# Performance work log

Hardware: AMD Instinct MI355X
Metric: run time of the kernel (lower is better)

Reference implementation:

```python
import jax, jax.numpy as jnp
import numpy as np

EPS = 1e-9


def setup_inputs() -> dict:
    key = jax.random.key(0)
    k1, k2, k3 = jax.random.split(key, 3)
    B, N, E, F_IN, F_OUT = 8, 2048, 1024, 256, 256
    x = jax.random.normal(k1, (B, N, F_IN), dtype=jnp.float32)
    H = jax.random.uniform(k2, (B, N, E), dtype=jnp.float32)  # soft incidence matrix
    weight = jax.random.normal(k3, (F_IN, F_OUT), dtype=jnp.float32) * (1.0 / np.sqrt(F_OUT))
    return {"x": x, "H": H, "weight": weight}


def reference(x, H, weight):
    # x: [B, N, Fin], H: [B, N, E], weight: [Fin, Fout]
    # Torch builds diag_embed(Dv_inv)/diag_embed(De_inv) and uses dense bmm;
    # mathematically identical to elementwise row-scaling, done here directly.
    Dv = jnp.sum(H, axis=2)                       # [B, N]  (= bmm(H, ones))
    De = jnp.sum(H, axis=1)                       # [B, E]
    Dv_inv = 1.0 / (Dv + EPS)
    De_inv = 1.0 / (De + EPS)
    xw = jnp.matmul(x, weight)                    # [B, N, Fout]
    HTX = jnp.einsum('bne,bnf->bef', H, xw)       # H^T @ X
    HDeHTX = jnp.einsum('bne,bef->bnf', H, De_inv[:, :, None] * HTX)
    out = Dv_inv[:, :, None] * HDeHTX             # [B, N, Fout]
    # dropout in eval mode (identity); relu kept
    return jax.nn.relu(out)
```

## Files before the change

### kernel.cpp

```cpp
#include <hip/hip_runtime.h>
#include <stdint.h>


typedef __bf16 bf16x8 __attribute__((ext_vector_type(8)));
typedef float f32x4 __attribute__((ext_vector_type(4)));

#define PADK 72

__device__ __forceinline__ uint16_t f2b(float f) {
  __bf16 h = (__bf16)f;
  return __builtin_bit_cast(uint16_t, h);
}

__device__ __forceinline__ f32x4 mfma16(bf16x8 a, bf16x8 b, f32x4 c) {
  return __builtin_amdgcn_mfma_f32_16x16x32_bf16(a, b, c, 0, 0, 0);
}

__device__ __forceinline__ void gload16(const void* src, void* dst) {
  __builtin_amdgcn_global_load_lds(
      (const __attribute__((address_space(1))) void*)src,
      (__attribute__((address_space(3))) void*)dst, 16, 0, 0);
}

#define PIPE_WAIT4() do { \
    asm volatile("s_waitcnt vmcnt(4)" ::: "memory"); \
    __builtin_amdgcn_s_barrier(); \
    __builtin_amdgcn_sched_barrier(0); \
  } while (0)
#define PIPE_WAIT0() do { \
    asm volatile("s_waitcnt vmcnt(0)" ::: "memory"); \
    __builtin_amdgcn_s_barrier(); \
    __builtin_amdgcn_sched_barrier(0); \
  } while (0)

__global__ __launch_bounds__(256) void k_prep_w(const float* __restrict__ W,
    uint16_t* __restrict__ Wt) {
  __shared__ __align__(16) uint16_t T[64 * 68];
  const int k0 = blockIdx.x * 64, f0 = blockIdx.y * 64;
  const int t = threadIdx.x;
  const int r0 = (t >> 4) * 4, cc = (t & 15) * 4;
  float vv[4][4];
  #pragma unroll
  for (int i = 0; i < 4; ++i) {
    float4 q = *(const float4*)(W + (size_t)(k0 + r0 + i) * 256 + f0 + cc);
    vv[i][0] = q.x; vv[i][1] = q.y; vv[i][2] = q.z; vv[i][3] = q.w;
  }
  #pragma unroll
  for (int j = 0; j < 4; ++j) {
    union { uint16_t s[4]; uint2 u; } p;
    #pragma unroll
    for (int i = 0; i < 4; ++i) p.s[i] = f2b(vv[i][j]);
    *(uint2*)&T[(cc + j) * 68 + r0] = p.u;
  }
  __syncthreads();
  const int er = t >> 2, c2 = (t & 3) * 16;
  union { uint16_t s[16]; uint4 q[2]; } o;
  #pragma unroll
  for (int m = 0; m < 4; ++m)
    *(uint2*)&o.s[m * 4] = *(const uint2*)&T[er * 68 + c2 + m * 4];
  uint16_t* dst = Wt + (size_t)(f0 + er) * 256 + k0 + c2;
  *(uint4*)dst = o.q[0];
  *(uint4*)(dst + 8) = o.q[1];
}

__global__ __launch_bounds__(256) void k_phase1(const float* __restrict__ H,
    const float* __restrict__ X, const uint16_t* __restrict__ Wt,
    uint16_t* __restrict__ Hbt, uint16_t* __restrict__ Hb,
    float* __restrict__ DvPart, float* __restrict__ DePart,
    uint16_t* __restrict__ XWt) {
  __shared__ __align__(16) unsigned char smem[25600];
  const int lin = blockIdx.x;
  const int t = threadIdx.x, lane = t & 63, wave = t >> 6;

  if (lin < 512) {
    uint16_t* As = (uint16_t*)smem;
    uint16_t* Bs = (uint16_t*)(smem + 16384);
    const int n0 = (lin & 31) * 64, f0 = ((lin >> 5) & 1) * 128, b = lin >> 6;
    const int l15 = lane & 15, lq = lane >> 4;
    const int rlane = lane >> 3;
    const int srcswz = ((lane & 7) ^ rlane) << 3;
    const uint16_t* Ag = Wt + (size_t)f0 * 256;
    const int br = t >> 2, kc = (t & 3) * 16;
    const float* Xg = X + ((size_t)b * 2048 + n0 + br) * 256 + kc;
    f32x4 acc[4][2] = {};
    for (int kt = 0; kt < 4; ++kt) {
      if (kt) __syncthreads();
      const int k0 = kt * 64;
      #pragma unroll
      for (int i = 0; i < 4; ++i) {
        const int r = wave * 32 + i * 8;
        gload16(Ag + (size_t)(r + rlane) * 256 + k0 + srcswz, As + r * 64);
      }
      {
        float4 RX[4];
        const float* s = Xg + k0;
        #pragma unroll
        for (int q = 0; q < 4; ++q) RX[q] = *(const float4*)(s + q * 4);
        uint16_t* d = Bs + br * PADK + kc;
        const float* f = (const float*)RX;
        #pragma unroll
        for (int q = 0; q < 2; ++q) {
          union { uint16_t s[8]; uint4 u; } p;
          #pragma unroll
          for (int j = 0; j < 8; ++j) p.s[j] = f2b(f[q * 8 + j]);
          *(uint4*)(d + q * 8) = p.u;
        }
      }
      __syncthreads();
      #pragma unroll
      for (int h = 0; h < 2; ++h) {
        bf16x8 af[4], bf[2];
        #pragma unroll
        for (int i = 0; i < 4; ++i) {
          const int r = (wave >> 1) * 64 + i * 16 + l15;
          af[i] = *(const bf16x8*)(As + r * 64 + ((((h << 2) | lq) ^ (r & 7)) << 3));
        }
        #pragma unroll
        for (int j = 0; j < 2; ++j) {
          const int r = (wave & 1) * 32 + j * 16 + l15;
          bf[j] = *(const bf16x8*)(Bs + r * PADK + h * 32 + lq * 8);
        }
        #pragma unroll
        for (int i = 0; i < 4; ++i)
          #pragma unroll
          for (int j = 0; j < 2; ++j)
            acc[i][j] = mfma16(af[i], bf[j], acc[i][j]);
      }
    }
    #pragma unroll
    for (int i = 0; i < 4; ++i) {
      const int fr = f0 + (wave >> 1) * 64 + i * 16 + lq * 4;
      #pragma unroll
      for (int j = 0; j < 2; ++j) {
        const int col = n0 + (wave & 1) * 32 + j * 16 + l15;
        #pragma unroll
        for (int reg = 0; reg < 4; ++reg)
          XWt[((size_t)b * 256 + fr + reg) * 2048 + col] = f2b(acc[i][j][reg]);
      }
    }
  } else {
    uint16_t* T = (uint16_t*)smem;
    float* cs = (float*)(smem + 8704);
    const int l2 = lin - 512;
    const int n0 = (l2 & 31) * 64, e0 = ((l2 >> 5) & 15) * 64, b = l2 >> 9;
    const int r0 = (t >> 4) * 4;
    const int cc = (t & 15) * 4;
    float vv[4][4];
    float dv[4];
    float de0 = 0.f, de1 = 0.f, de2 = 0.f, de3 = 0.f;
    #pragma unroll
    for (int i = 0; i < 4; ++i) {
      float4 q = *(const float4*)(H + ((size_t)b * 2048 + n0 + r0 + i) * 1024 + e0 + cc);
      vv[i][0] = q.x; vv[i][1] = q.y; vv[i][2] = q.z; vv[i][3] = q.w;
      float rs = (q.x + q.y) + (q.z + q.w);
      rs += __shfl_xor(rs, 1); rs += __shfl_xor(rs, 2);
      rs += __shfl_xor(rs, 4); rs += __shfl_xor(rs, 8);
      dv[i] = rs;
      de0 += q.x; de1 += q.y; de2 += q.z; de3 += q.w;
    }
    #pragma unroll
    for (int i = 0; i < 4; ++i) {
      union { uint16_t s[4]; uint2 u; } p;
      #pragma unroll
      for (int j = 0; j < 4; ++j) p.s[j] = f2b(vv[i][j]);
      *(uint2*)(Hb + ((size_t)b * 2048 + n0 + r0 + i) * 1024 + e0 + cc) = p.u;
    }
    #pragma unroll
    for (int j = 0; j < 4; ++j) {
      union { uint16_t s[4]; uint2 u; } p;
      #pragma unroll
      for (int i = 0; i < 4; ++i) p.s[i] = f2b(vv[i][j]);
      *(uint2*)&T[(cc + j) * 68 + r0] = p.u;
    }
    de0 += __shfl_xor(de0, 16); de0 += __shfl_xor(de0, 32);
    de1 += __shfl_xor(de1, 16); de1 += __shfl_xor(de1, 32);
    de2 += __shfl_xor(de2, 16); de2 += __shfl_xor(de2, 32);
    de3 += __shfl_xor(de3, 16); de3 += __shfl_xor(de3, 32);
    if (lane < 16) *(float4*)&cs[wave * 64 + cc] = make_float4(de0, de1, de2, de3);
    if ((lane & 15) == 0) {
      #pragma unroll
      for (int i = 0; i < 4; ++i)
        DvPart[((size_t)b * 2048 + n0 + r0 + i) * 16 + ((l2 >> 5) & 15)] = dv[i];
    }
    __syncthreads();
    const int er = t >> 2, c2 = (t & 3) * 16;
    union { uint16_t s[16]; uint4 q[2]; } o;
    #pragma unroll
    for (int m = 0; m < 4; ++m)
      *(uint2*)&o.s[m * 4] = *(const uint2*)&T[er * 68 + c2 + m * 4];
    uint16_t* dst = Hbt + ((size_t)b * 1024 + e0 + er) * 2048 + n0 + c2;
    *(uint4*)dst = o.q[0];
    *(uint4*)(dst + 8) = o.q[1];
    if (t < 64) {
      float s = (cs[0 * 64 + t] + cs[1 * 64 + t]) + (cs[2 * 64 + t] + cs[3 * 64 + t]);
      DePart[((size_t)b * 1024 + e0 + t) * 32 + (l2 & 31)] = s;
    }
  }
}

__global__ __launch_bounds__(256) void k_gemm2(const uint16_t* __restrict__ Hbt,
    const uint16_t* __restrict__ XWt, const float* __restrict__ DePart,
    uint16_t* __restrict__ Yt) {
  __shared__ __align__(16) uint16_t As[3][64 * 64];
  __shared__ __align__(16) uint16_t Bs[3][64 * 64];
  __shared__ float sde[64];
  const int e0 = blockIdx.x * 64, f0 = blockIdx.y * 64, b = blockIdx.z;
  const int t = threadIdx.x, lane = t & 63, wave = t >> 6;
  const int l15 = lane & 15, lq = lane >> 4;
  const int rlane = lane >> 3;
  const int srcswz = ((lane & 7) ^ rlane) << 3;
  const uint16_t* Ag = XWt + ((size_t)b * 256 + f0) * 2048;
  const uint16_t* Bg = Hbt + ((size_t)b * 1024 + e0) * 2048;
  auto stage = [&](uint16_t* Ad, uint16_t* Bd, int kt) {
    const int k0 = kt * 64;
    #pragma unroll
    for (int i = 0; i < 2; ++i) {
      const int r = wave * 16 + i * 8;
      gload16(Ag + (size_t)(r + rlane) * 2048 + k0 + srcswz, Ad + r * 64);
      gload16(Bg + (size_t)(r + rlane) * 2048 + k0 + srcswz, Bd + r * 64);
    }
  };
  f32x4 acc[2][2] = {};
  auto compute = [&](const uint16_t* Ad, const uint16_t* Bd) {
    #pragma unroll
    for (int h = 0; h < 2; ++h) {
      bf16x8 af[2], bf[2];
      #pragma unroll
      for (int i = 0; i < 2; ++i) {
        const int r = (wave >> 1) * 32 + i * 16 + l15;
        af[i] = *(const bf16x8*)(Ad + r * 64 + ((((h << 2) | lq) ^ (r & 7)) << 3));
      }
      #pragma unroll
      for (int j = 0; j < 2; ++j) {
        const int r = (wave & 1) * 32 + j * 16 + l15;
        bf[j] = *(const bf16x8*)(Bd + r * 64 + ((((h << 2) | lq) ^ (r & 7)) << 3));
      }
      #pragma unroll
      for (int i = 0; i < 2; ++i)
        #pragma unroll
        for (int j = 0; j < 2; ++j)
          acc[i][j] = mfma16(af[i], bf[j], acc[i][j]);
    }
  };
  if (t < 64) {
    const float* p = DePart + ((size_t)b * 1024 + e0 + t) * 32;
    float4 a0 = *(const float4*)(p + 0),  a1 = *(const float4*)(p + 4);
    float4 a2 = *(const float4*)(p + 8),  a3 = *(const float4*)(p + 12);
    float4 a4 = *(const float4*)(p + 16), a5 = *(const float4*)(p + 20);
    float4 a6 = *(const float4*)(p + 24), a7 = *(const float4*)(p + 28);
    float s = (((a0.x + a0.y) + (a0.z + a0.w)) + ((a1.x + a1.y) + (a1.z + a1.w)))
            + (((a2.x + a2.y) + (a2.z + a2.w)) + ((a3.x + a3.y) + (a3.z + a3.w)))
            + ((((a4.x + a4.y) + (a4.z + a4.w)) + ((a5.x + a5.y) + (a5.z + a5.w)))
            + (((a6.x + a6.y) + (a6.z + a6.w)) + ((a7.x + a7.y) + (a7.z + a7.w))));
    sde[t] = 1.f / (s + 1e-9f);
  }
  stage(As[0], Bs[0], 0);
  stage(As[1], Bs[1], 1);
  __syncthreads();
  const int NT = 32;
  uint16_t *cA = As[0], *nA = As[1], *fA = As[2];
  uint16_t *cB = Bs[0], *nB = Bs[1], *fB = Bs[2];
  for (int kt = 0; kt < NT - 2; ++kt) {
    stage(fA, fB, kt + 2);
    compute(cA, cB);
    PIPE_WAIT4();
    uint16_t* t1 = cA; cA = nA; nA = fA; fA = t1;
    uint16_t* t2 = cB; cB = nB; nB = fB; fB = t2;
  }
  compute(cA, cB);
  PIPE_WAIT0();
  compute(nA, nB);
  #pragma unroll
  for (int i = 0; i < 2; ++i) {
    const int fr = f0 + (wave >> 1) * 32 + i * 16 + lq * 4;
    #pragma unroll
    for (int j = 0; j < 2; ++j) {
      const int el = (wave & 1) * 32 + j * 16 + l15;
      const float sc = sde[el];
      uint16_t* dst = Yt + ((size_t)b * 256 + fr) * 1024 + e0 + el;
      #pragma unroll
      for (int reg = 0; reg < 4; ++reg)
        dst[(size_t)reg * 1024] = f2b(acc[i][j][reg] * sc);
    }
  }
}

__global__ __launch_bounds__(256) void k_gemm3(const uint16_t* __restrict__ Hb,
    const uint16_t* __restrict__ Yt, const float* __restrict__ DvPart,
    float* __restrict__ out) {
  __shared__ __align__(16) uint16_t As[3][64 * 64];
  __shared__ __align__(16) uint16_t Bs[3][64 * 64];
  __shared__ float sdv[64];
  const int n0 = blockIdx.x * 64, f0 = blockIdx.y * 64, b = blockIdx.z;
  const int t = threadIdx.x, lane = t & 63, wave = t >> 6;
  const int l15 = lane & 15, lq = lane >> 4;
  const int rlane = lane >> 3;
  const int srcswz = ((lane & 7) ^ rlane) << 3;
  const uint16_t* Ag = Hb + ((size_t)b * 2048 + n0) * 1024;
  const uint16_t* Bg = Yt + ((size_t)b * 256 + f0) * 1024;
  auto stage = [&](uint16_t* Ad, uint16_t* Bd, int kt) {
    const int k0 = kt * 64;
    #pragma unroll
    for (int i = 0; i < 2; ++i) {
      const int r = wave * 16 + i * 8;
      gload16(Ag + (size_t)(r + rlane) * 1024 + k0 + srcswz, Ad + r * 64);
      gload16(Bg + (size_t)(r + rlane) * 1024 + k0 + srcswz, Bd + r * 64);
    }
  };
  f32x4 acc[2][2] = {};
  auto compute = [&](const uint16_t* Ad, const uint16_t* Bd) {
    #pragma unroll
    for (int h = 0; h < 2; ++h) {
      bf16x8 af[2], bf[2];
      #pragma unroll
      for (int i = 0; i < 2; ++i) {
        const int r = (wave >> 1) * 32 + i * 16 + l15;
        af[i] = *(const bf16x8*)(Ad + r * 64 + ((((h << 2) | lq) ^ (r & 7)) << 3));
      }
      #pragma unroll
      for (int j = 0; j < 2; ++j) {
        const int r = (wave & 1) * 32 + j * 16 + l15;
        bf[j] = *(const bf16x8*)(Bd + r * 64 + ((((h << 2) | lq) ^ (r & 7)) << 3));
      }
      #pragma unroll
      for (int i = 0; i < 2; ++i)
        #pragma unroll
        for (int j = 0; j < 2; ++j)
          acc[i][j] = mfma16(af[i], bf[j], acc[i][j]);
    }
  };
  if (t < 64) {
    const float* p = DvPart + ((size_t)b * 2048 + n0 + t) * 16;
    float4 a0 = *(const float4*)(p + 0),  a1 = *(const float4*)(p + 4);
    float4 a2 = *(const float4*)(p + 8),  a3 = *(const float4*)(p + 12);
    float s = (((a0.x + a0.y) + (a0.z + a0.w)) + ((a1.x + a1.y) + (a1.z + a1.w)))
            + (((a2.x + a2.y) + (a2.z + a2.w)) + ((a3.x + a3.y) + (a3.z + a3.w)));
    sdv[t] = 1.f / (s + 1e-9f);
  }
  stage(As[0], Bs[0], 0);
  stage(As[1], Bs[1], 1);
  __syncthreads();
  const int NT = 16;
  uint16_t *cA = As[0], *nA = As[1], *fA = As[2];
  uint16_t *cB = Bs[0], *nB = Bs[1], *fB = Bs[2];
  for (int kt = 0; kt < NT - 2; ++kt) {
    stage(fA, fB, kt + 2);
    compute(cA, cB);
    PIPE_WAIT4();
    uint16_t* t1 = cA; cA = nA; nA = fA; fA = t1;
    uint16_t* t2 = cB; cB = nB; nB = fB; fB = t2;
  }
  compute(cA, cB);
  PIPE_WAIT0();
  compute(nA, nB);
  #pragma unroll
  for (int i = 0; i < 2; ++i) {
    const int nl = (wave >> 1) * 32 + i * 16 + lq * 4;
    #pragma unroll
    for (int reg = 0; reg < 4; ++reg) {
      const int row = n0 + nl + reg;
      const float sc = sdv[nl + reg];
      #pragma unroll
      for (int j = 0; j < 2; ++j) {
        const int col = f0 + (wave & 1) * 32 + j * 16 + l15;
        const float v = acc[i][j][reg] * sc;
        out[((size_t)b * 2048 + row) * 256 + col] = v > 0.f ? v : 0.f;
      }
    }
  }
}

extern "C" void kernel_launch(void* const* d_in, const int* in_sizes, int n_in,
                              void* d_out, int out_size, void* d_ws, size_t ws_size,
                              hipStream_t stream) {
  (void)in_sizes; (void)n_in; (void)out_size;
  const float* x = (const float*)d_in[0];
  const float* H = (const float*)d_in[1];
  const float* W = (const float*)d_in[2];
  float* out = (float*)d_out;

  if (ws_size < 81920000) return;
  char* ws = (char*)d_ws;
  uint16_t* Hbt    = (uint16_t*)(ws);
  uint16_t* Hb     = (uint16_t*)(ws + 33554432);
  uint16_t* XWt    = (uint16_t*)(ws + 67108864);
  uint16_t* Yt     = (uint16_t*)(ws + 75497472);
  float*    DvPart = (float*)(ws + 79691776);
  float*    DePart = (float*)(ws + 80740352);
  uint16_t* Wt     = (uint16_t*)(ws + 81788928);

  k_prep_w<<<dim3(4, 4),     256, 0, stream>>>(W, Wt);
  k_phase1<<<dim3(4608),     256, 0, stream>>>(H, x, Wt, Hbt, Hb, DvPart, DePart, XWt);
  k_gemm2 <<<dim3(16, 4, 8), 256, 0, stream>>>(Hbt, XWt, DePart, Yt);
  k_gemm3 <<<dim3(32, 4, 8), 256, 0, stream>>>(Hb, Yt, DvPart, out);
}
```

Before: 76.46 us.

## Rebalance phase1: H blocks process two E tiles, XW GEMM tiles shrink

The fused phase-1 kernel now schedules the H conversion blocks first, and each one handles two 64-wide E tiles (128 columns). That halves the H block count and the Dv partial count, so k_gemm3 reads 8 partials instead of 16. The XW GEMM blocks shrink from 128x64 to 64x64 output tiles, doubling their count to 1024 and cutting LDS use. The goal is better load balance, with the memory-bound H work launched first and less per-block overhead. The cost is higher register pressure in the H path and more redundant X loads in the GEMM.

Result: no change. 77.01 us (+0.7%).

```diff
diff --git a/kernel.cpp b/kernel.cpp
--- a/kernel.cpp
+++ b/kernel.cpp
@@ -4,8 +4,6 @@
 
 typedef __bf16 bf16x8 __attribute__((ext_vector_type(8)));
 typedef float f32x4 __attribute__((ext_vector_type(4)));
-
-#define PADK 72
 
 __device__ __forceinline__ uint16_t f2b(float f) {
   __bf16 h = (__bf16)f;
@@ -68,27 +66,131 @@
     uint16_t* __restrict__ Hbt, uint16_t* __restrict__ Hb,
     float* __restrict__ DvPart, float* __restrict__ DePart,
     uint16_t* __restrict__ XWt) {
-  __shared__ __align__(16) unsigned char smem[25600];
+  __shared__ __align__(16) unsigned char smem[20480];
   const int lin = blockIdx.x;
   const int t = threadIdx.x, lane = t & 63, wave = t >> 6;
 
-  if (lin < 512) {
+  if (lin < 2048) {
+    uint16_t* T0 = (uint16_t*)smem;
+    uint16_t* T1 = (uint16_t*)(smem + 9216);
+    float* cs = (float*)(smem + 18432);
+    const int n0 = (lin & 31) * 64, ep = (lin >> 5) & 7, b = lin >> 8;
+    const int e0a = ep * 128, e0b = e0a + 64;
+    const int r0 = (t >> 4) * 4;
+    const int cc = (t & 15) * 4;
+    float4 q0[4], q1[4];
+    #pragma unroll
+    for (int i = 0; i < 4; ++i)
+      q0[i] = *(const float4*)(H + ((size_t)b * 2048 + n0 + r0 + i) * 1024 + e0a + cc);
+    #pragma unroll
+    for (int i = 0; i < 4; ++i)
+      q1[i] = *(const float4*)(H + ((size_t)b * 2048 + n0 + r0 + i) * 1024 + e0b + cc);
+    float dv[4];
+    {
+      float de0 = 0.f, de1 = 0.f, de2 = 0.f, de3 = 0.f;
+      #pragma unroll
+      for (int i = 0; i < 4; ++i) {
+        float4 q = q0[i];
+        float rs = (q.x + q.y) + (q.z + q.w);
+        rs += __shfl_xor(rs, 1); rs += __shfl_xor(rs, 2);
+        rs += __shfl_xor(rs, 4); rs += __shfl_xor(rs, 8);
+        dv[i] = rs;
+        de0 += q.x; de1 += q.y; de2 += q.z; de3 += q.w;
+        union { uint16_t s[4]; uint2 u; } p;
+        p.s[0] = f2b(q.x); p.s[1] = f2b(q.y); p.s[2] = f2b(q.z); p.s[3] = f2b(q.w);
+        *(uint2*)(Hb + ((size_t)b * 2048 + n0 + r0 + i) * 1024 + e0a + cc) = p.u;
+      }
+      #pragma unroll
+      for (int j = 0; j < 4; ++j) {
+        union { uint16_t s[4]; uint2 u; } p;
+        p.s[0] = f2b(((const float*)&q0[0])[j]);
+        p.s[1] = f2b(((const float*)&q0[1])[j]);
+        p.s[2] = f2b(((const float*)&q0[2])[j]);
+        p.s[3] = f2b(((const float*)&q0[3])[j]);
+        *(uint2*)&T0[(cc + j) * 72 + r0] = p.u;
+      }
+      de0 += __shfl_xor(de0, 16); de0 += __shfl_xor(de0, 32);
+      de1 += __shfl_xor(de1, 16); de1 += __shfl_xor(de1, 32);
+      de2 += __shfl_xor(de2, 16); de2 += __shfl_xor(de2, 32);
+      de3 += __shfl_xor(de3, 16); de3 += __shfl_xor(de3, 32);
+      if (lane < 16) *(float4*)&cs[(0 * 4 + wave) * 64 + cc] = make_float4(de0, de1, de2, de3);
+    }
+    {
+      float de0 = 0.f, de1 = 0.f, de2 = 0.f, de3 = 0.f;
+      #pragma unroll
+      for (int i = 0; i < 4; ++i) {
+        float4 q = q1[i];
+        float rs = (q.x + q.y) + (q.z + q.w);
+        rs += __shfl_xor(rs, 1); rs += __shfl_xor(rs, 2);
+        rs += __shfl_xor(rs, 4); rs += __shfl_xor(rs, 8);
+        dv[i] += rs;
+        de0 += q.x; de1 += q.y; de2 += q.z; de3 += q.w;
+        union { uint16_t s[4]; uint2 u; } p;
+        p.s[0] = f2b(q.x); p.s[1] = f2b(q.y); p.s[2] = f2b(q.z); p.s[3] = f2b(q.w);
+        *(uint2*)(Hb + ((size_t)b * 2048 + n0 + r0 + i) * 1024 + e0b + cc) = p.u;
+      }
+      #pragma unroll
+      for (int j = 0; j < 4; ++j) {
+        union { uint16_t s[4]; uint2 u; } p;
+        p.s[0] = f2b(((const float*)&q1[0])[j]);
+        p.s[1] = f2b(((const float*)&q1[1])[j]);
+        p.s[2] = f2b(((const float*)&q1[2])[j]);
+        p.s[3] = f2b(((const float*)&q1[3])[j]);
+        *(uint2*)&T1[(cc + j) * 72 + r0] = p.u;
+      }
+      de0 += __shfl_xor(de0, 16); de0 += __shfl_xor(de0, 32);
+      de1 += __shfl_xor(de1, 16); de1 += __shfl_xor(de1, 32);
+      de2 += __shfl_xor(de2, 16); de2 += __shfl_xor(de2, 32);
+      de3 += __shfl_xor(de3, 16); de3 += __shfl_xor(de3, 32);
+      if (lane < 16) *(float4*)&cs[(1 * 4 + wave) * 64 + cc] = make_float4(de0, de1, de2, de3);
+    }
+    if ((lane & 15) == 0) {
+      #pragma unroll
+      for (int i = 0; i < 4; ++i)
+        DvPart[((size_t)b * 2048 + n0 + r0 + i) * 8 + ep] = dv[i];
+    }
+    __syncthreads();
+    const int er = t >> 2, c2 = (t & 3) * 16;
+    {
+      uint4 o0 = *(const uint4*)&T0[er * 72 + c2];
+      uint4 o1 = *(const uint4*)&T0[er * 72 + c2 + 8];
+      uint16_t* dst = Hbt + ((size_t)b * 1024 + e0a + er) * 2048 + n0 + c2;
+      *(uint4*)dst = o0;
+      *(uint4*)(dst + 8) = o1;
+    }
+    {
+      uint4 o0 = *(const uint4*)&T1[er * 72 + c2];
+      uint4 o1 = *(const uint4*)&T1[er * 72 + c2 + 8];
+      uint16_t* dst = Hbt + ((size_t)b * 1024 + e0b + er) * 2048 + n0 + c2;
+      *(uint4*)dst = o0;
+      *(uint4*)(dst + 8) = o1;
+    }
+    if (t < 64) {
+      float s = (cs[0 * 64 + t] + cs[1 * 64 + t]) + (cs[2 * 64 + t] + cs[3 * 64 + t]);
+      DePart[((size_t)b * 1024 + e0a + t) * 32 + (lin & 31)] = s;
+    } else if (t < 128) {
+      const int t2 = t - 64;
+      float s = (cs[4 * 64 + t2] + cs[5 * 64 + t2]) + (cs[6 * 64 + t2] + cs[7 * 64 + t2]);
+      DePart[((size_t)b * 1024 + e0b + t2) * 32 + (lin & 31)] = s;
+    }
+  } else {
     uint16_t* As = (uint16_t*)smem;
-    uint16_t* Bs = (uint16_t*)(smem + 16384);
-    const int n0 = (lin & 31) * 64, f0 = ((lin >> 5) & 1) * 128, b = lin >> 6;
+    uint16_t* Bs = (uint16_t*)(smem + 8192);
+    const int l1 = lin - 2048;
+    const int n0 = (l1 & 31) * 64, f0 = ((l1 >> 5) & 3) * 64, b = l1 >> 7;
     const int l15 = lane & 15, lq = lane >> 4;
     const int rlane = lane >> 3;
     const int srcswz = ((lane & 7) ^ rlane) << 3;
     const uint16_t* Ag = Wt + (size_t)f0 * 256;
     const int br = t >> 2, kc = (t & 3) * 16;
     const float* Xg = X + ((size_t)b * 2048 + n0 + br) * 256 + kc;
-    f32x4 acc[4][2] = {};
+    f32x4 acc[2][2] = {};
     for (int kt = 0; kt < 4; ++kt) {
       if (kt) __syncthreads();
       const int k0 = kt * 64;
       #pragma unroll
-      for (int i = 0; i < 4; ++i) {
-        const int r = wave * 32 + i * 8;
+      for (int i = 0; i < 2; ++i) {
+        const int r = wave * 16 + i * 8;
         gload16(Ag + (size_t)(r + rlane) * 256 + k0 + srcswz, As + r * 64);
       }
       {
@@ -96,7 +198,7 @@
         const float* s = Xg + k0;
         #pragma unroll
         for (int q = 0; q < 4; ++q) RX[q] = *(const float4*)(s + q * 4);
-        uint16_t* d = Bs + br * PADK + kc;
+        uint16_t* d = Bs + br * 72 + kc;
         const float* f = (const float*)RX;
         #pragma unroll
         for (int q = 0; q < 2; ++q) {
@@ -109,27 +211,27 @@
       __syncthreads();
       #pragma unroll
       for (int h = 0; h < 2; ++h) {
-        bf16x8 af[4], bf[2];
-        #pragma unroll
-        for (int i = 0; i < 4; ++i) {
-          const int r = (wave >> 1) * 64 + i * 16 + l15;
+        bf16x8 af[2], bf[2];
+        #pragma unroll
+        for (int i = 0; i < 2; ++i) {
+          const int r = (wave >> 1) * 32 + i * 16 + l15;
           af[i] = *(const bf16x8*)(As + r * 64 + ((((h << 2) | lq) ^ (r & 7)) << 3));
         }
         #pragma unroll
         for (int j = 0; j < 2; ++j) {
           const int r = (wave & 1) * 32 + j * 16 + l15;
-          bf[j] = *(const bf16x8*)(Bs + r * PADK + h * 32 + lq * 8);
+          bf[j] = *(const bf16x8*)(Bs + r * 72 + h * 32 + lq * 8);
         }
         #pragma unroll
-        for (int i = 0; i < 4; ++i)
+        for (int i = 0; i < 2; ++i)
           #pragma unroll
           for (int j = 0; j < 2; ++j)
             acc[i][j] = mfma16(af[i], bf[j], acc[i][j]);
       }
     }
     #pragma unroll
-    for (int i = 0; i < 4; ++i) {
-      const int fr = f0 + (wave >> 1) * 64 + i * 16 + lq * 4;
+    for (int i = 0; i < 2; ++i) {
+      const int fr = f0 + (wave >> 1) * 32 + i * 16 + lq * 4;
       #pragma unroll
       for (int j = 0; j < 2; ++j) {
         const int col = n0 + (wave & 1) * 32 + j * 16 + l15;
@@ -137,63 +239,6 @@
         for (int reg = 0; reg < 4; ++reg)
           XWt[((size_t)b * 256 + fr + reg) * 2048 + col] = f2b(acc[i][j][reg]);
       }
-    }
-  } else {
-    uint16_t* T = (uint16_t*)smem;
-    float* cs = (float*)(smem + 8704);
-    const int l2 = lin - 512;
-    const int n0 = (l2 & 31) * 64, e0 = ((l2 >> 5) & 15) * 64, b = l2 >> 9;
-    const int r0 = (t >> 4) * 4;
-    const int cc = (t & 15) * 4;
-    float vv[4][4];
-    float dv[4];
-    float de0 = 0.f, de1 = 0.f, de2 = 0.f, de3 = 0.f;
-    #pragma unroll
-    for (int i = 0; i < 4; ++i) {
-      float4 q = *(const float4*)(H + ((size_t)b * 2048 + n0 + r0 + i) * 1024 + e0 + cc);
-      vv[i][0] = q.x; vv[i][1] = q.y; vv[i][2] = q.z; vv[i][3] = q.w;
-      float rs = (q.x + q.y) + (q.z + q.w);
-      rs += __shfl_xor(rs, 1); rs += __shfl_xor(rs, 2);
-      rs += __shfl_xor(rs, 4); rs += __shfl_xor(rs, 8);
-      dv[i] = rs;
-      de0 += q.x; de1 += q.y; de2 += q.z; de3 += q.w;
-    }
-    #pragma unroll
-    for (int i = 0; i < 4; ++i) {
-      union { uint16_t s[4]; uint2 u; } p;
-      #pragma unroll
-      for (int j = 0; j < 4; ++j) p.s[j] = f2b(vv[i][j]);
-      *(uint2*)(Hb + ((size_t)b * 2048 + n0 + r0 + i) * 1024 + e0 + cc) = p.u;
-    }
-    #pragma unroll
-    for (int j = 0; j < 4; ++j) {
-      union { uint16_t s[4]; uint2 u; } p;
-      #pragma unroll
-      for (int i = 0; i < 4; ++i) p.s[i] = f2b(vv[i][j]);
-      *(uint2*)&T[(cc + j) * 68 + r0] = p.u;
-    }
-    de0 += __shfl_xor(de0, 16); de0 += __shfl_xor(de0, 32);
-    de1 += __shfl_xor(de1, 16); de1 += __shfl_xor(de1, 32);
-    de2 += __shfl_xor(de2, 16); de2 += __shfl_xor(de2, 32);
-    de3 += __shfl_xor(de3, 16); de3 += __shfl_xor(de3, 32);
-    if (lane < 16) *(float4*)&cs[wave * 64 + cc] = make_float4(de0, de1, de2, de3);
-    if ((lane & 15) == 0) {
-      #pragma unroll
-      for (int i = 0; i < 4; ++i)
-        DvPart[((size_t)b * 2048 + n0 + r0 + i) * 16 + ((l2 >> 5) & 15)] = dv[i];
-    }
-    __syncthreads();
-    const int er = t >> 2, c2 = (t & 3) * 16;
-    union { uint16_t s[16]; uint4 q[2]; } o;
-    #pragma unroll
-    for (int m = 0; m < 4; ++m)
-      *(uint2*)&o.s[m * 4] = *(const uint2*)&T[er * 68 + c2 + m * 4];
-    uint16_t* dst = Hbt + ((size_t)b * 1024 + e0 + er) * 2048 + n0 + c2;
-    *(uint4*)dst = o.q[0];
-    *(uint4*)(dst + 8) = o.q[1];
-    if (t < 64) {
-      float s = (cs[0 * 64 + t] + cs[1 * 64 + t]) + (cs[2 * 64 + t] + cs[3 * 64 + t]);
-      DePart[((size_t)b * 1024 + e0 + t) * 32 + (l2 & 31)] = s;
     }
   }
 }
@@ -330,11 +375,9 @@
     }
   };
   if (t < 64) {
-    const float* p = DvPart + ((size_t)b * 2048 + n0 + t) * 16;
-    float4 a0 = *(const float4*)(p + 0),  a1 = *(const float4*)(p + 4);
-    float4 a2 = *(const float4*)(p + 8),  a3 = *(const float4*)(p + 12);
-    float s = (((a0.x + a0.y) + (a0.z + a0.w)) + ((a1.x + a1.y) + (a1.z + a1.w)))
-            + (((a2.x + a2.y) + (a2.z + a2.w)) + ((a3.x + a3.y) + (a3.z + a3.w)));
+    const float* p = DvPart + ((size_t)b * 2048 + n0 + t) * 8;
+    float4 a0 = *(const float4*)(p + 0), a1 = *(const float4*)(p + 4);
+    float s = (((a0.x + a0.y) + (a0.z + a0.w)) + ((a1.x + a1.y) + (a1.z + a1.w)));
     sdv[t] = 1.f / (s + 1e-9f);
   }
   stage(As[0], Bs[0], 0);
@@ -390,7 +433,7 @@
   uint16_t* Wt     = (uint16_t*)(ws + 81788928);
 
   k_prep_w<<<dim3(4, 4),     256, 0, stream>>>(W, Wt);
-  k_phase1<<<dim3(4608),     256, 0, stream>>>(H, x, Wt, Hbt, Hb, DvPart, DePart, XWt);
+  k_phase1<<<dim3(3072),     256, 0, stream>>>(H, x, Wt, Hbt, Hb, DvPart, DePart, XWt);
   k_gemm2 <<<dim3(16, 4, 8), 256, 0, stream>>>(Hbt, XWt, DePart, Yt);
   k_gemm3 <<<dim3(32, 4, 8), 256, 0, stream>>>(Hb, Yt, DvPart, out);
 }
```

## Drop transposed H copy; transpose H tiles in LDS inside gemm2

Applied to the files above, without the earlier changes.

Phase1 no longer writes a transposed bf16 copy of H. It streams H in row blocks, writing only Hb, and computes the final DvInv directly along with per-block De partials. gemm2 now reads Hb row-major through registers and transposes each tile into padded LDS, with a register double-buffered pipeline driven by explicit waitcnt and barriers. The XW GEMM is retiled to 64x64 blocks. This saves 32MB of global writes and the workspace, at the cost of extra LDS transpose work and narrower 8-byte loads in gemm2.

After: 88.44 us. 15.7% more time.

```diff
diff --git a/kernel.cpp b/kernel.cpp
--- a/kernel.cpp
+++ b/kernel.cpp
@@ -4,8 +4,6 @@
 
 typedef __bf16 bf16x8 __attribute__((ext_vector_type(8)));
 typedef float f32x4 __attribute__((ext_vector_type(4)));
-
-#define PADK 72
 
 __device__ __forceinline__ uint16_t f2b(float f) {
   __bf16 h = (__bf16)f;
@@ -65,30 +63,61 @@
 
 __global__ __launch_bounds__(256) void k_phase1(const float* __restrict__ H,
     const float* __restrict__ X, const uint16_t* __restrict__ Wt,
-    uint16_t* __restrict__ Hbt, uint16_t* __restrict__ Hb,
-    float* __restrict__ DvPart, float* __restrict__ DePart,
-    uint16_t* __restrict__ XWt) {
-  __shared__ __align__(16) unsigned char smem[25600];
+    uint16_t* __restrict__ Hb, float* __restrict__ DvInv,
+    float* __restrict__ DePart, uint16_t* __restrict__ XWt) {
+  __shared__ __align__(16) unsigned char smem[17408];
   const int lin = blockIdx.x;
   const int t = threadIdx.x, lane = t & 63, wave = t >> 6;
 
-  if (lin < 512) {
+  if (lin < 1024) {
+    float* dvp = (float*)smem;
+    const int nb = lin & 127, b = lin >> 7;
+    const int n0 = nb * 16;
+    const float* Hrow = H + ((size_t)b * 2048 + n0) * 1024 + t * 4;
+    uint16_t* HbRow = Hb + ((size_t)b * 2048 + n0) * 1024 + t * 4;
+    float de0 = 0.f, de1 = 0.f, de2 = 0.f, de3 = 0.f;
+    float4 qn = *(const float4*)(Hrow);
+    #pragma unroll
+    for (int i = 0; i < 16; ++i) {
+      float4 q = qn;
+      if (i < 15) qn = *(const float4*)(Hrow + (size_t)(i + 1) * 1024);
+      de0 += q.x; de1 += q.y; de2 += q.z; de3 += q.w;
+      float rs = (q.x + q.y) + (q.z + q.w);
+      rs += __shfl_xor(rs, 1);  rs += __shfl_xor(rs, 2);
+      rs += __shfl_xor(rs, 4);  rs += __shfl_xor(rs, 8);
+      rs += __shfl_xor(rs, 16); rs += __shfl_xor(rs, 32);
+      if (lane == 0) dvp[i * 4 + wave] = rs;
+      union { uint16_t s[4]; uint2 u; } p;
+      p.s[0] = f2b(q.x); p.s[1] = f2b(q.y); p.s[2] = f2b(q.z); p.s[3] = f2b(q.w);
+      *(uint2*)(HbRow + (size_t)i * 1024) = p.u;
+    }
+    {
+      float* dp = DePart + ((size_t)b * 1024 + t * 4) * 128 + nb;
+      dp[0] = de0; dp[128] = de1; dp[256] = de2; dp[384] = de3;
+    }
+    __syncthreads();
+    if (t < 16) {
+      float s = (dvp[t * 4 + 0] + dvp[t * 4 + 1]) + (dvp[t * 4 + 2] + dvp[t * 4 + 3]);
+      DvInv[b * 2048 + n0 + t] = 1.f / (s + 1e-9f);
+    }
+  } else {
     uint16_t* As = (uint16_t*)smem;
-    uint16_t* Bs = (uint16_t*)(smem + 16384);
-    const int n0 = (lin & 31) * 64, f0 = ((lin >> 5) & 1) * 128, b = lin >> 6;
+    uint16_t* Bs = (uint16_t*)(smem + 8192);
+    const int l1 = lin - 1024;
+    const int n0 = (l1 & 31) * 64, f0 = ((l1 >> 5) & 3) * 64, b = l1 >> 7;
     const int l15 = lane & 15, lq = lane >> 4;
     const int rlane = lane >> 3;
     const int srcswz = ((lane & 7) ^ rlane) << 3;
     const uint16_t* Ag = Wt + (size_t)f0 * 256;
     const int br = t >> 2, kc = (t & 3) * 16;
     const float* Xg = X + ((size_t)b * 2048 + n0 + br) * 256 + kc;
-    f32x4 acc[4][2] = {};
+    f32x4 acc[2][2] = {};
     for (int kt = 0; kt < 4; ++kt) {
       if (kt) __syncthreads();
       const int k0 = kt * 64;
       #pragma unroll
-      for (int i = 0; i < 4; ++i) {
-        const int r = wave * 32 + i * 8;
+      for (int i = 0; i < 2; ++i) {
+        const int r = wave * 16 + i * 8;
         gload16(Ag + (size_t)(r + rlane) * 256 + k0 + srcswz, As + r * 64);
       }
       {
@@ -96,7 +125,7 @@
         const float* s = Xg + k0;
         #pragma unroll
         for (int q = 0; q < 4; ++q) RX[q] = *(const float4*)(s + q * 4);
-        uint16_t* d = Bs + br * PADK + kc;
+        uint16_t* d = Bs + br * 72 + kc;
         const float* f = (const float*)RX;
         #pragma unroll
         for (int q = 0; q < 2; ++q) {
@@ -109,27 +138,27 @@
       __syncthreads();
       #pragma unroll
       for (int h = 0; h < 2; ++h) {
-        bf16x8 af[4], bf[2];
-        #pragma unroll
-        for (int i = 0; i < 4; ++i) {
-          const int r = (wave >> 1) * 64 + i * 16 + l15;
+        bf16x8 af[2], bf[2];
+        #pragma unroll
+        for (int i = 0; i < 2; ++i) {
+          const int r = (wave >> 1) * 32 + i * 16 + l15;
           af[i] = *(const bf16x8*)(As + r * 64 + ((((h << 2) | lq) ^ (r & 7)) << 3));
         }
         #pragma unroll
         for (int j = 0; j < 2; ++j) {
           const int r = (wave & 1) * 32 + j * 16 + l15;
-          bf[j] = *(const bf16x8*)(Bs + r * PADK + h * 32 + lq * 8);
+          bf[j] = *(const bf16x8*)(Bs + r * 72 + h * 32 + lq * 8);
         }
         #pragma unroll
-        for (int i = 0; i < 4; ++i)
+        for (int i = 0; i < 2; ++i)
           #pragma unroll
           for (int j = 0; j < 2; ++j)
             acc[i][j] = mfma16(af[i], bf[j], acc[i][j]);
       }
     }
     #pragma unroll
-    for (int i = 0; i < 4; ++i) {
-      const int fr = f0 + (wave >> 1) * 64 + i * 16 + lq * 4;
+    for (int i = 0; i < 2; ++i) {
+      const int fr = f0 + (wave >> 1) * 32 + i * 16 + lq * 4;
       #pragma unroll
       for (int j = 0; j < 2; ++j) {
         const int col = n0 + (wave & 1) * 32 + j * 16 + l15;
@@ -138,71 +167,15 @@
           XWt[((size_t)b * 256 + fr + reg) * 2048 + col] = f2b(acc[i][j][reg]);
       }
     }
-  } else {
-    uint16_t* T = (uint16_t*)smem;
-    float* cs = (float*)(smem + 8704);
-    const int l2 = lin - 512;
-    const int n0 = (l2 & 31) * 64, e0 = ((l2 >> 5) & 15) * 64, b = l2 >> 9;
-    const int r0 = (t >> 4) * 4;
-    const int cc = (t & 15) * 4;
-    float vv[4][4];
-    float dv[4];
-    float de0 = 0.f, de1 = 0.f, de2 = 0.f, de3 = 0.f;
-    #pragma unroll
-    for (int i = 0; i < 4; ++i) {
-      float4 q = *(const float4*)(H + ((size_t)b * 2048 + n0 + r0 + i) * 1024 + e0 + cc);
-      vv[i][0] = q.x; vv[i][1] = q.y; vv[i][2] = q.z; vv[i][3] = q.w;
-      float rs = (q.x + q.y) + (q.z + q.w);
-      rs += __shfl_xor(rs, 1); rs += __shfl_xor(rs, 2);
-      rs += __shfl_xor(rs, 4); rs += __shfl_xor(rs, 8);
-      dv[i] = rs;
-      de0 += q.x; de1 += q.y; de2 += q.z; de3 += q.w;
-    }
-    #pragma unroll
-    for (int i = 0; i < 4; ++i) {
-      union { uint16_t s[4]; uint2 u; } p;
-      #pragma unroll
-      for (int j = 0; j < 4; ++j) p.s[j] = f2b(vv[i][j]);
-      *(uint2*)(Hb + ((size_t)b * 2048 + n0 + r0 + i) * 1024 + e0 + cc) = p.u;
-    }
-    #pragma unroll
-    for (int j = 0; j < 4; ++j) {
-      union { uint16_t s[4]; uint2 u; } p;
-      #pragma unroll
-      for (int i = 0; i < 4; ++i) p.s[i] = f2b(vv[i][j]);
-      *(uint2*)&T[(cc + j) * 68 + r0] = p.u;
-    }
-    de0 += __shfl_xor(de0, 16); de0 += __shfl_xor(de0, 32);
-    de1 += __shfl_xor(de1, 16); de1 += __shfl_xor(de1, 32);
-    de2 += __shfl_xor(de2, 16); de2 += __shfl_xor(de2, 32);
-    de3 += __shfl_xor(de3, 16); de3 += __shfl_xor(de3, 32);
-    if (lane < 16) *(float4*)&cs[wave * 64 + cc] = make_float4(de0, de1, de2, de3);
-    if ((lane & 15) == 0) {
-      #pragma unroll
-      for (int i = 0; i < 4; ++i)
-        DvPart[((size_t)b * 2048 + n0 + r0 + i) * 16 + ((l2 >> 5) & 15)] = dv[i];
-    }
-    __syncthreads();
-    const int er = t >> 2, c2 = (t & 3) * 16;
-    union { uint16_t s[16]; uint4 q[2]; } o;
-    #pragma unroll
-    for (int m = 0; m < 4; ++m)
-      *(uint2*)&o.s[m * 4] = *(const uint2*)&T[er * 68 + c2 + m * 4];
-    uint16_t* dst = Hbt + ((size_t)b * 1024 + e0 + er) * 2048 + n0 + c2;
-    *(uint4*)dst = o.q[0];
-    *(uint4*)(dst + 8) = o.q[1];
-    if (t < 64) {
-      float s = (cs[0 * 64 + t] + cs[1 * 64 + t]) + (cs[2 * 64 + t] + cs[3 * 64 + t]);
-      DePart[((size_t)b * 1024 + e0 + t) * 32 + (l2 & 31)] = s;
-    }
-  }
-}
-
-__global__ __launch_bounds__(256) void k_gemm2(const uint16_t* __restrict__ Hbt,
+  }
+}
+
+__global__ __launch_bounds__(256) void k_gemm2(const uint16_t* __restrict__ Hb,
     const uint16_t* __restrict__ XWt, const float* __restrict__ DePart,
     uint16_t* __restrict__ Yt) {
   __shared__ __align__(16) uint16_t As[3][64 * 64];
-  __shared__ __align__(16) uint16_t Bs[3][64 * 64];
+  __shared__ __align__(16) uint16_t Bsm[2][64 * 72];
+  __shared__ float sde4[64][4];
   __shared__ float sde[64];
   const int e0 = blockIdx.x * 64, f0 = blockIdx.y * 64, b = blockIdx.z;
   const int t = threadIdx.x, lane = t & 63, wave = t >> 6;
@@ -210,14 +183,29 @@
   const int rlane = lane >> 3;
   const int srcswz = ((lane & 7) ^ rlane) << 3;
   const uint16_t* Ag = XWt + ((size_t)b * 256 + f0) * 2048;
-  const uint16_t* Bg = Hbt + ((size_t)b * 1024 + e0) * 2048;
-  auto stage = [&](uint16_t* Ad, uint16_t* Bd, int kt) {
+  const int br0 = (t >> 4) * 4;
+  const int bcc = (t & 15) * 4;
+  const uint16_t* Bgb = Hb + (size_t)b * 2048 * 1024 + e0 + bcc;
+  auto stageA = [&](uint16_t* Ad, int kt) {
     const int k0 = kt * 64;
     #pragma unroll
     for (int i = 0; i < 2; ++i) {
       const int r = wave * 16 + i * 8;
       gload16(Ag + (size_t)(r + rlane) * 2048 + k0 + srcswz, Ad + r * 64);
-      gload16(Bg + (size_t)(r + rlane) * 2048 + k0 + srcswz, Bd + r * 64);
+    }
+  };
+  auto loadB = [&](uint2* R, int kt) {
+    const uint16_t* s = Bgb + (size_t)(kt * 64 + br0) * 1024;
+    #pragma unroll
+    for (int i = 0; i < 4; ++i) R[i] = *(const uint2*)(s + (size_t)i * 1024);
+  };
+  auto writeB = [&](uint16_t* Bd, const uint2* R) {
+    #pragma unroll
+    for (int j = 0; j < 4; ++j) {
+      union { uint16_t s[4]; uint2 u; } p;
+      #pragma unroll
+      for (int i = 0; i < 4; ++i) p.s[i] = ((const uint16_t*)&R[i])[j];
+      *(uint2*)&Bd[(bcc + j) * 72 + br0] = p.u;
     }
   };
   f32x4 acc[2][2] = {};
@@ -233,7 +221,7 @@
       #pragma unroll
       for (int j = 0; j < 2; ++j) {
         const int r = (wave & 1) * 32 + j * 16 + l15;
-        bf[j] = *(const bf16x8*)(Bd + r * 64 + ((((h << 2) | lq) ^ (r & 7)) << 3));
+        bf[j] = *(const bf16x8*)(Bd + r * 72 + h * 32 + lq * 8);
       }
       #pragma unroll
       for (int i = 0; i < 2; ++i)
@@ -242,34 +230,54 @@
           acc[i][j] = mfma16(af[i], bf[j], acc[i][j]);
     }
   };
-  if (t < 64) {
-    const float* p = DePart + ((size_t)b * 1024 + e0 + t) * 32;
-    float4 a0 = *(const float4*)(p + 0),  a1 = *(const float4*)(p + 4);
-    float4 a2 = *(const float4*)(p + 8),  a3 = *(const float4*)(p + 12);
-    float4 a4 = *(const float4*)(p + 16), a5 = *(const float4*)(p + 20);
-    float4 a6 = *(const float4*)(p + 24), a7 = *(const float4*)(p + 28);
-    float s = (((a0.x + a0.y) + (a0.z + a0.w)) + ((a1.x + a1.y) + (a1.z + a1.w)))
-            + (((a2.x + a2.y) + (a2.z + a2.w)) + ((a3.x + a3.y) + (a3.z + a3.w)))
-            + ((((a4.x + a4.y) + (a4.z + a4.w)) + ((a5.x + a5.y) + (a5.z + a5.w)))
-            + (((a6.x + a6.y) + (a6.z + a6.w)) + ((a7.x + a7.y) + (a7.z + a7.w))));
-    sde[t] = 1.f / (s + 1e-9f);
-  }
-  stage(As[0], Bs[0], 0);
-  stage(As[1], Bs[1], 1);
-  __syncthreads();
+  {
+    const float* p = DePart + ((size_t)b * 1024 + e0 + (t & 63)) * 128 + (t >> 6) * 32;
+    float s = 0.f;
+    #pragma unroll
+    for (int q = 0; q < 8; ++q) {
+      float4 a = *(const float4*)(p + q * 4);
+      s += (a.x + a.y) + (a.z + a.w);
+    }
+    sde4[t & 63][t >> 6] = s;
+  }
+  uint2 RB0[4], RB1[4];
+  loadB(RB0, 0);
+  stageA(As[0], 0);
+  stageA(As[1], 1);
+  asm volatile("s_waitcnt vmcnt(4)" ::: "memory");
+  writeB(Bsm[0], RB0);
+  loadB(RB1, 1);
+  asm volatile("s_waitcnt vmcnt(6) lgkmcnt(0)" ::: "memory");
+  __builtin_amdgcn_s_barrier();
+  __builtin_amdgcn_sched_barrier(0);
+  if (t < 64)
+    sde[t] = 1.f / (((sde4[t][0] + sde4[t][1]) + (sde4[t][2] + sde4[t][3])) + 1e-9f);
   const int NT = 32;
   uint16_t *cA = As[0], *nA = As[1], *fA = As[2];
-  uint16_t *cB = Bs[0], *nB = Bs[1], *fB = Bs[2];
-  for (int kt = 0; kt < NT - 2; ++kt) {
-    stage(fA, fB, kt + 2);
-    compute(cA, cB);
-    PIPE_WAIT4();
-    uint16_t* t1 = cA; cA = nA; nA = fA; fA = t1;
-    uint16_t* t2 = cB; cB = nB; nB = fB; fB = t2;
-  }
-  compute(cA, cB);
-  PIPE_WAIT0();
-  compute(nA, nB);
+  #define G2_STEP(KT, RBH, RBF, BSC, BSN)                                    \
+    do {                                                                     \
+      stageA(fA, (KT) + 2);                                                  \
+      loadB(RBF, (KT) + 2);                                                  \
+      compute(cA, BSC);                                                      \
+      asm volatile("s_waitcnt vmcnt(6)" ::: "memory");                       \
+      writeB(BSN, RBH);                                                      \
+      asm volatile("s_waitcnt lgkmcnt(0)" ::: "memory");                     \
+      __builtin_amdgcn_s_barrier();                                          \
+      __builtin_amdgcn_sched_barrier(0);                                     \
+      uint16_t* tp = cA; cA = nA; nA = fA; fA = tp;                          \
+    } while (0)
+  for (int kt = 0; kt < NT - 2; kt += 2) {
+    G2_STEP(kt,     RB1, RB0, Bsm[0], Bsm[1]);
+    G2_STEP(kt + 1, RB0, RB1, Bsm[1], Bsm[0]);
+  }
+  #undef G2_STEP
+  compute(cA, Bsm[0]);
+  asm volatile("s_waitcnt vmcnt(0)" ::: "memory");
+  writeB(Bsm[1], RB1);
+  asm volatile("s_waitcnt lgkmcnt(0)" ::: "memory");
+  __builtin_amdgcn_s_barrier();
+  __builtin_amdgcn_sched_barrier(0);
+  compute(nA, Bsm[1]);
   #pragma unroll
   for (int i = 0; i < 2; ++i) {
     const int fr = f0 + (wave >> 1) * 32 + i * 16 + lq * 4;
@@ -286,7 +294,7 @@
 }
 
 __global__ __launch_bounds__(256) void k_gemm3(const uint16_t* __restrict__ Hb,
-    const uint16_t* __restrict__ Yt, const float* __restrict__ DvPart,
+    const uint16_t* __restrict__ Yt, const float* __restrict__ DvInv,
     float* __restrict__ out) {
   __shared__ __align__(16) uint16_t As[3][64 * 64];
   __shared__ __align__(16) uint16_t Bs[3][64 * 64];
@@ -329,14 +337,7 @@
           acc[i][j] = mfma16(af[i], bf[j], acc[i][j]);
     }
   };
-  if (t < 64) {
-    const float* p = DvPart + ((size_t)b * 2048 + n0 + t) * 16;
-    float4 a0 = *(const float4*)(p + 0),  a1 = *(const float4*)(p + 4);
-    float4 a2 = *(const float4*)(p + 8),  a3 = *(const float4*)(p + 12);
-    float s = (((a0.x + a0.y) + (a0.z + a0.w)) + ((a1.x + a1.y) + (a1.z + a1.w)))
-            + (((a2.x + a2.y) + (a2.z + a2.w)) + ((a3.x + a3.y) + (a3.z + a3.w)));
-    sdv[t] = 1.f / (s + 1e-9f);
-  }
+  if (t < 64) sdv[t] = DvInv[b * 2048 + n0 + t];
   stage(As[0], Bs[0], 0);
   stage(As[1], Bs[1], 1);
   __syncthreads();
@@ -379,18 +380,17 @@
   const float* W = (const float*)d_in[2];
   float* out = (float*)d_out;
 
-  if (ws_size < 81920000) return;
+  if (ws_size < 50528256) return;
   char* ws = (char*)d_ws;
-  uint16_t* Hbt    = (uint16_t*)(ws);
-  uint16_t* Hb     = (uint16_t*)(ws + 33554432);
-  uint16_t* XWt    = (uint16_t*)(ws + 67108864);
-  uint16_t* Yt     = (uint16_t*)(ws + 75497472);
-  float*    DvPart = (float*)(ws + 79691776);
-  float*    DePart = (float*)(ws + 80740352);
-  uint16_t* Wt     = (uint16_t*)(ws + 81788928);
+  uint16_t* Hb     = (uint16_t*)(ws);
+  uint16_t* XWt    = (uint16_t*)(ws + 33554432);
+  uint16_t* Yt     = (uint16_t*)(ws + 41943040);
+  float*    DvInv  = (float*)(ws + 46137344);
+  float*    DePart = (float*)(ws + 46202880);
+  uint16_t* Wt     = (uint16_t*)(ws + 50397184);
 
   k_prep_w<<<dim3(4, 4),     256, 0, stream>>>(W, Wt);
-  k_phase1<<<dim3(4608),     256, 0, stream>>>(H, x, Wt, Hbt, Hb, DvPart, DePart, XWt);
-  k_gemm2 <<<dim3(16, 4, 8), 256, 0, stream>>>(Hbt, XWt, DePart, Yt);
-  k_gemm3 <<<dim3(32, 4, 8), 256, 0, stream>>>(Hb, Yt, DvPart, out);
-}
+  k_phase1<<<dim3(2048),     256, 0, stream>>>(H, x, Wt, Hb, DvInv, DePart, XWt);
+  k_gemm2 <<<dim3(16, 4, 8), 256, 0, stream>>>(Hb, XWt, DePart, Yt);
+  k_gemm3 <<<dim3(32, 4, 8), 256, 0, stream>>>(Hb, Yt, DvInv, out);
+}
```
